# Kernel tuning notes

Hardware: AMD Instinct MI355X
Metric: run time of the kernel (lower is better)

Reference implementation:

```python
import jax, jax.numpy as jnp
import numpy as np

B, N, M, D, H, K, V = 2, 2048, 2048, 1024, 16, 64, 64
MAX_WAVELENGTH = 10000
SCALE_FACTOR = 1.0


def rope(x, positions, max_wavelength, scale_factor):
    # x: [b, s, h, k]; positions: [b, s] int
    head_dim = x.shape[-1]
    fraction = 2.0 * jnp.arange(head_dim // 2, dtype=x.dtype) / head_dim
    timescale = jnp.asarray(max_wavelength, x.dtype) ** fraction            # [k/2]
    # scaled positions -> phase per (b, s, 1 head bcast, k/2)
    phase = (positions.astype(x.dtype) / scale_factor)[:, :, None, None] / timescale  # [b,s,1,k/2]
    sin, cos = jnp.sin(phase), jnp.cos(phase)
    x1, x2 = jnp.split(x, 2, axis=-1)
    return jnp.concatenate([x1 * cos - x2 * sin, x2 * cos + x1 * sin], axis=-1)


def setup_inputs() -> dict:
    key = jax.random.key(0)
    ks = jax.random.split(key, 8)
    scale = 1.0 / np.sqrt(D)  # keep logits numerically sane with random params
    inp = {
        "query": jax.random.normal(ks[0], (B, N, D), jnp.float32),
        "q_positions": jnp.broadcast_to(jnp.arange(N, dtype=jnp.int32), (B, N)),
        "key": jax.random.normal(ks[1], (B, M, D), jnp.float32),
        "k_positions": jnp.broadcast_to(jnp.arange(M, dtype=jnp.int32), (B, M)),
        "value": jax.random.normal(ks[2], (B, M, D), jnp.float32),
        "mask": jnp.ones((1, 1, N, M), dtype=bool),
        "P_q": jax.random.normal(ks[3], (H, D, K), jnp.float32) * scale,
        "P_k": jax.random.normal(ks[4], (H, D, K), jnp.float32) * scale,
        "P_v": jax.random.normal(ks[5], (H, D, V), jnp.float32) * scale,
        "P_o": jax.random.normal(ks[6], (H, D, V), jnp.float32) * scale,
    }
    return inp


def reference(query, q_positions, key, k_positions, value, mask, P_q, P_k, P_v, P_o):
    q = jnp.einsum('bnd,hdk->bnhk', query, P_q)
    k = jnp.einsum('bmd,hdk->bmhk', key, P_k)
    v = jnp.einsum('bmd,hdv->bmhv', value, P_v)
    q = rope(q, q_positions, MAX_WAVELENGTH, SCALE_FACTOR)
    k = rope(k, k_positions, MAX_WAVELENGTH, SCALE_FACTOR)
    logits = jnp.einsum('bnhk,bmhk->bhnm', q, k)
    if mask is not None:
        logits = jnp.where(mask, logits, -jnp.inf)
    weights = jax.nn.softmax(logits, axis=-1)
    o = jnp.einsum('bhnm,bmhv->bnhv', weights, v)
    return jnp.einsum('bnhv,hdv->bnd', o, P_o)
```

## Files before the change

kernel.cpp:

```cpp
#include <hip/hip_runtime.h>
#include <hip/hip_bf16.h>
#include <math.h>

#define B_ 2
#define N_ 2048
#define M_ 2048
#define D_ 1024
#define H_ 16


typedef _Float16 f16;
typedef f16  f16x4 __attribute__((ext_vector_type(4)));
typedef f16  f16x8 __attribute__((ext_vector_type(8)));
typedef float f32x4  __attribute__((ext_vector_type(4)));
typedef float f32x16 __attribute__((ext_vector_type(16)));

#define MFMA16(a, b, c) __builtin_amdgcn_mfma_f32_16x16x32_f16((a), (b), (c), 0, 0, 0)
#define MFMA32(a, b, c) __builtin_amdgcn_mfma_f32_32x32x16_f16((a), (b), (c), 0, 0, 0)
#define LDST 72

__global__ __launch_bounds__(256) void prep_all(
    const float* __restrict__ Pq, const float* __restrict__ Pk,
    const float* __restrict__ Pv, const float* __restrict__ Po,
    const int* __restrict__ qpos, const int* __restrict__ kpos,
    f16* __restrict__ Ptq, f16* __restrict__ Ptk, f16* __restrict__ Ptv,
    f16* __restrict__ Wo, float2* __restrict__ tabq, float2* __restrict__ tabk)
{
  __shared__ float Ts[64][65];
  const int z = blockIdx.y, x = blockIdx.x, tid = threadIdx.x;
  if (z < 3) {
    if (x >= 256) return;
    const float* P = (z == 0) ? Pq : (z == 1) ? Pk : Pv;
    f16* Pt = (z == 0) ? Ptq : (z == 1) ? Ptk : Ptv;
    const int d0 = (x & 15) * 64, h = x >> 4;
    #pragma unroll
    for (int it = 0; it < 4; ++it) {
      int fi = tid + 256 * it;
      int dr = fi >> 4, c4 = (fi & 15) << 2;
      float4 v = *(const float4*)(P + ((size_t)h * D_ + d0 + dr) * 64 + c4);
      Ts[dr][c4+0] = v.x; Ts[dr][c4+1] = v.y; Ts[dr][c4+2] = v.z; Ts[dr][c4+3] = v.w;
    }
    __syncthreads();
    const int c = tid >> 2, dp = (tid & 3) * 16;
    f16x8 w0, w1;
    #pragma unroll
    for (int i = 0; i < 8; ++i) { w0[i] = (f16)Ts[dp + i][c]; w1[i] = (f16)Ts[dp + 8 + i][c]; }
    f16* dst = Pt + ((size_t)h * 64 + c) * D_ + d0 + dp;
    *(f16x8*)dst = w0;
    *(f16x8*)(dst + 8) = w1;
  } else if (z == 3) {
    int e = (x * 256 + tid) * 4;
    if (e >= H_ * D_ * 64) return;
    int h = e >> 16, d = (e >> 6) & 1023, v = e & 63;
    float4 xx = *(const float4*)(Po + e);
    f16x4 w = {(f16)xx.x, (f16)xx.y, (f16)xx.z, (f16)xx.w};
    *(f16x4*)&Wo[(size_t)d * 1024 + h * 64 + v] = w;
  } else {
    if (x >= 512) return;
    int idx = x * 256 + tid;
    int r = idx >> 5, c = idx & 31;
    const int* pos = (z == 4) ? qpos : kpos;
    float2* tab = (z == 4) ? tabq : tabk;
    float fpos = (float)pos[r];
    float inv_ts = exp2f(-(float)c * 0.4152410118609203f);
    float ph = fpos * inv_ts, sn, cs;
    sincosf(ph, &sn, &cs);
    tab[idx] = make_float2(cs, sn);
  }
}

__global__ __launch_bounds__(256) void gemm_fused(
    const float* __restrict__ Aq, const float* __restrict__ Ak,
    const float* __restrict__ Av,
    const f16* __restrict__ Bq, const f16* __restrict__ Bk,
    const f16* __restrict__ Bv,
    const float2* __restrict__ tabq, const float2* __restrict__ tabk,
    f16* __restrict__ dq, f16* __restrict__ dk, f16* __restrict__ dv)
{
  __shared__ f16 As[128 * LDST];
  __shared__ f16 Bs[128 * LDST];
  const int tid = threadIdx.x, lane = tid & 63, wave = tid >> 6;
  const int quad = lane >> 4, l16 = lane & 15;
  const int col0 = blockIdx.x * 128, row0 = blockIdx.y * 128;
  const int op = blockIdx.z;
  const int wr = (wave >> 1) * 64, wc = (wave & 1) * 64;

  const float* A  = (op == 0) ? Aq : (op == 1) ? Ak : Av;
  const f16*  Bt  = (op == 0) ? Bq : (op == 1) ? Bk : Bv;

  f32x4 acc[4][4] = {};
  float4 apre[8];
  f16x8  bpre[4];

  #pragma unroll
  for (int it = 0; it < 8; ++it) {
    int fi = tid + 256 * it;
    int row = fi >> 4, c4 = (fi & 15) << 2;
    apre[it] = *(const float4*)(A + (size_t)(row0 + row) * 1024 + c4);
  }
  #pragma unroll
  for (int it = 0; it < 4; ++it) {
    int fi = tid + 256 * it;
    int row = fi >> 3, c8 = (fi & 7) * 8;
    bpre[it] = *(const f16x8*)(Bt + (size_t)(col0 + row) * 1024 + c8);
  }

  for (int k0 = 0; k0 < 1024; k0 += 64) {
    __syncthreads();
    #pragma unroll
    for (int it = 0; it < 8; ++it) {
      int fi = tid + 256 * it;
      int row = fi >> 4, c4 = (fi & 15) << 2;
      f16x4 hv = {(f16)apre[it].x, (f16)apre[it].y, (f16)apre[it].z, (f16)apre[it].w};
      *(f16x4*)&As[row * LDST + c4] = hv;
    }
    #pragma unroll
    for (int it = 0; it < 4; ++it) {
      int fi = tid + 256 * it;
      int row = fi >> 3, c8 = (fi & 7) * 8;
      *(f16x8*)&Bs[row * LDST + c8] = bpre[it];
    }
    __syncthreads();
    if (k0 + 64 < 1024) {
      #pragma unroll
      for (int it = 0; it < 8; ++it) {
        int fi = tid + 256 * it;
        int row = fi >> 4, c4 = (fi & 15) << 2;
        apre[it] = *(const float4*)(A + (size_t)(row0 + row) * 1024 + k0 + 64 + c4);
      }
      #pragma unroll
      for (int it = 0; it < 4; ++it) {
        int fi = tid + 256 * it;
        int row = fi >> 3, c8 = (fi & 7) * 8;
        bpre[it] = *(const f16x8*)(Bt + (size_t)(col0 + row) * 1024 + k0 + 64 + c8);
      }
    }
    #pragma unroll
    for (int ks = 0; ks < 2; ++ks) {
      f16x8 af[4], bf[4];
      #pragma unroll
      for (int i = 0; i < 4; ++i)
        af[i] = *(const f16x8*)&As[(wr + i * 16 + l16) * LDST + ks * 32 + quad * 8];
      #pragma unroll
      for (int j = 0; j < 4; ++j)
        bf[j] = *(const f16x8*)&Bs[(wc + j * 16 + l16) * LDST + ks * 32 + quad * 8];
      #pragma unroll
      for (int i = 0; i < 4; ++i)
        #pragma unroll
        for (int j = 0; j < 4; ++j)
          acc[i][j] = MFMA16(af[i], bf[j], acc[i][j]);
    }
  }

  if (op == 2) {
    #pragma unroll
    for (int i = 0; i < 4; ++i) {
      int r = row0 + wr + i * 16 + quad * 4;
      int b = r >> 11, s = r & 2047;
      #pragma unroll
      for (int j = 0; j < 4; ++j) {
        int col = col0 + wc + j * 16 + l16;
        int h = col >> 6, v = col & 63;
        f16x4 w = {(f16)acc[i][j][0], (f16)acc[i][j][1],
                   (f16)acc[i][j][2], (f16)acc[i][j][3]};
        *(f16x4*)&dv[((size_t)(b * H_ + h) * 64 + v) * 2048 + s] = w;
      }
    }
  } else {
    const float2* tab = (op == 0) ? tabq : tabk;
    f16* oq = (op == 0) ? dq : dk;
    #pragma unroll
    for (int i = 0; i < 4; ++i) {
      #pragma unroll
      for (int reg = 0; reg < 4; ++reg) {
        int r = row0 + wr + i * 16 + quad * 4 + reg;
        int b = r >> 11, s = r & 2047;
        #pragma unroll
        for (int j = 0; j < 2; ++j) {
          int col = col0 + wc + j * 16 + l16;
          int h = col >> 6, c = col & 63;
          float2 cs = tab[r * 32 + c];
          float x1 = acc[i][j][reg], x2 = acc[i][j + 2][reg];
          size_t base = ((size_t)(b * H_ + h) * 2048 + s) * 64;
          oq[base + c]      = (f16)(x1 * cs.x - x2 * cs.y);
          oq[base + c + 32] = (f16)(x2 * cs.x + x1 * cs.y);
        }
      }
    }
  }
}

__global__ __launch_bounds__(256) void flash5(
    const f16* __restrict__ q, const f16* __restrict__ k,
    const f16* __restrict__ vt, f16* __restrict__ o)
{
  __shared__ f16 Ks[64 * LDST];
  __shared__ f16 Vts[64 * LDST];
  __shared__ f16 Ps[4][32 * LDST];

  const int tid = threadIdx.x, lane = tid & 63, wave = tid >> 6;
  const int L = lane >> 5, nl = lane & 31;
  const int n0 = blockIdx.x * 128;
  const int h = blockIdx.y, b = blockIdx.z;

  const f16* qb = q  + (size_t)(b * H_ + h) * N_ * 64;
  const f16* kb = k  + (size_t)(b * H_ + h) * M_ * 64;
  const f16* vb = vt + (size_t)(b * H_ + h) * 64 * M_;

  f16x8 qf[4];
  #pragma unroll
  for (int g = 0; g < 4; ++g)
    qf[g] = *(const f16x8*)(qb + (size_t)(n0 + wave * 32 + nl) * 64 + g * 16 + L * 8);

  f32x16 acc[2] = {};
  float mst = -INFINITY;
  float lst = 0.f;
  const float L2E = 1.4426950408889634f;

  const int srow = tid >> 2, soff = (tid & 3) * 16;
  f16* psw = Ps[wave];

  f16x8 kp0 = *(const f16x8*)(kb + (size_t)srow * 64 + soff);
  f16x8 kp1 = *(const f16x8*)(kb + (size_t)srow * 64 + soff + 8);
  f16x8 vp0 = *(const f16x8*)(vb + (size_t)srow * M_ + soff);
  f16x8 vp1 = *(const f16x8*)(vb + (size_t)srow * M_ + soff + 8);

  for (int m0 = 0; m0 < M_; m0 += 64) {
    __syncthreads();
    *(f16x8*)&Ks[srow * LDST + soff]      = kp0;
    *(f16x8*)&Ks[srow * LDST + soff + 8]  = kp1;
    *(f16x8*)&Vts[srow * LDST + soff]     = vp0;
    *(f16x8*)&Vts[srow * LDST + soff + 8] = vp1;
    __syncthreads();
    if (m0 + 64 < M_) {
      kp0 = *(const f16x8*)(kb + (size_t)(m0 + 64 + srow) * 64 + soff);
      kp1 = *(const f16x8*)(kb + (size_t)(m0 + 64 + srow) * 64 + soff + 8);
      vp0 = *(const f16x8*)(vb + (size_t)srow * M_ + m0 + 64 + soff);
      vp1 = *(const f16x8*)(vb + (size_t)srow * M_ + m0 + 64 + soff + 8);
    }

    f32x16 s[2] = {};
    #pragma unroll
    for (int u = 0; u < 2; ++u)
      #pragma unroll
      for (int g = 0; g < 4; ++g) {
        f16x8 af = *(const f16x8*)&Ks[(u * 32 + nl) * LDST + g * 16 + L * 8];
        s[u] = MFMA32(af, qf[g], s[u]);
      }

    float mx = s[0][0];
    #pragma unroll
    for (int u = 0; u < 2; ++u)
      #pragma unroll
      for (int r = 0; r < 16; ++r) mx = fmaxf(mx, s[u][r]);
    mx = fmaxf(mx, __shfl_xor(mx, 32));
    float m_new = fmaxf(mst, mx * L2E);
    bool chg = (m_new > mst);
    if (__ballot(chg)) {
      float alpha = exp2f(mst - m_new);
      #pragma unroll
      for (int u = 0; u < 2; ++u)
        #pragma unroll
        for (int r = 0; r < 16; ++r) acc[u][r] *= alpha;
      lst *= alpha;
    }
    mst = m_new;

    float sum = 0.f;
    float p[2][16];
    #pragma unroll
    for (int u = 0; u < 2; ++u)
      #pragma unroll
      for (int r = 0; r < 16; ++r) {
        float pv = exp2f(s[u][r] * L2E - m_new);
        p[u][r] = pv;
        sum += pv;
      }
    sum += __shfl_xor(sum, 32);
    lst += sum;

    #pragma unroll
    for (int u = 0; u < 2; ++u)
      #pragma unroll
      for (int rq = 0; rq < 4; ++rq) {
        f16x4 w = {(f16)p[u][rq * 4 + 0], (f16)p[u][rq * 4 + 1],
                   (f16)p[u][rq * 4 + 2], (f16)p[u][rq * 4 + 3]};
        *(f16x4*)&psw[nl * LDST + u * 32 + 8 * rq + 4 * L] = w;
      }
    f16x8 pb[4];
    #pragma unroll
    for (int g = 0; g < 4; ++g)
      pb[g] = *(const f16x8*)&psw[nl * LDST + g * 16 + L * 8];

    #pragma unroll
    for (int u = 0; u < 2; ++u)
      #pragma unroll
      for (int g = 0; g < 4; ++g) {
        f16x8 vf = *(const f16x8*)&Vts[(u * 32 + nl) * LDST + g * 16 + L * 8];
        acc[u] = MFMA32(vf, pb[g], acc[u]);
      }
  }

  float invl = 1.0f / lst;
  f16* ob = o + ((size_t)(b * N_ + n0 + wave * 32 + nl) * 1024) + h * 64;
  #pragma unroll
  for (int u = 0; u < 2; ++u)
    #pragma unroll
    for (int rq = 0; rq < 4; ++rq) {
      f16x4 w = {(f16)(acc[u][rq * 4 + 0] * invl), (f16)(acc[u][rq * 4 + 1] * invl),
                 (f16)(acc[u][rq * 4 + 2] * invl), (f16)(acc[u][rq * 4 + 3] * invl)};
      *(f16x4*)&ob[u * 32 + 8 * rq + 4 * L] = w;
    }
}

__global__ __launch_bounds__(256) void gemm_out(
    const f16* __restrict__ A, const f16* __restrict__ Bt,
    float* __restrict__ out)
{
  __shared__ f16 As[128 * LDST];
  __shared__ f16 Bs[64 * LDST];
  const int tid = threadIdx.x, lane = tid & 63, wave = tid >> 6;
  const int quad = lane >> 4, l16 = lane & 15;
  const int col0 = blockIdx.x * 64, row0 = blockIdx.y * 128;
  const int wr = (wave >> 1) * 64, wc = (wave & 1) * 32;

  f32x4 acc[4][2] = {};
  f16x8 apre[4], bpre[2];

  #pragma unroll
  for (int it = 0; it < 4; ++it) {
    int fi = tid + 256 * it;
    int row = fi >> 3, c8 = (fi & 7) * 8;
    apre[it] = *(const f16x8*)(A + (size_t)(row0 + row) * 1024 + c8);
  }
  #pragma unroll
  for (int it = 0; it < 2; ++it) {
    int fi = tid + 256 * it;
    int row = fi >> 3, c8 = (fi & 7) * 8;
    bpre[it] = *(const f16x8*)(Bt + (size_t)(col0 + row) * 1024 + c8);
  }

  for (int k0 = 0; k0 < 1024; k0 += 64) {
    __syncthreads();
    #pragma unroll
    for (int it = 0; it < 4; ++it) {
      int fi = tid + 256 * it;
      int row = fi >> 3, c8 = (fi & 7) * 8;
      *(f16x8*)&As[row * LDST + c8] = apre[it];
    }
    #pragma unroll
    for (int it = 0; it < 2; ++it) {
      int fi = tid + 256 * it;
      int row = fi >> 3, c8 = (fi & 7) * 8;
      *(f16x8*)&Bs[row * LDST + c8] = bpre[it];
    }
    __syncthreads();
    if (k0 + 64 < 1024) {
      #pragma unroll
      for (int it = 0; it < 4; ++it) {
        int fi = tid + 256 * it;
        int row = fi >> 3, c8 = (fi & 7) * 8;
        apre[it] = *(const f16x8*)(A + (size_t)(row0 + row) * 1024 + k0 + 64 + c8);
      }
      #pragma unroll
      for (int it = 0; it < 2; ++it) {
        int fi = tid + 256 * it;
        int row = fi >> 3, c8 = (fi & 7) * 8;
        bpre[it] = *(const f16x8*)(Bt + (size_t)(col0 + row) * 1024 + k0 + 64 + c8);
      }
    }
    #pragma unroll
    for (int ks = 0; ks < 2; ++ks) {
      f16x8 af[4], bf[2];
      #pragma unroll
      for (int i = 0; i < 4; ++i)
        af[i] = *(const f16x8*)&As[(wr + i * 16 + l16) * LDST + ks * 32 + quad * 8];
      #pragma unroll
      for (int j = 0; j < 2; ++j)
        bf[j] = *(const f16x8*)&Bs[(wc + j * 16 + l16) * LDST + ks * 32 + quad * 8];
      #pragma unroll
      for (int i = 0; i < 4; ++i)
        #pragma unroll
        for (int j = 0; j < 2; ++j)
          acc[i][j] = MFMA16(af[i], bf[j], acc[i][j]);
    }
  }

  #pragma unroll
  for (int i = 0; i < 4; ++i)
    #pragma unroll
    for (int j = 0; j < 2; ++j)
      #pragma unroll
      for (int reg = 0; reg < 4; ++reg)
        out[(size_t)(row0 + wr + i * 16 + quad * 4 + reg) * 1024 +
            col0 + wc + j * 16 + l16] = acc[i][j][reg];
}

extern "C" void kernel_launch(void* const* d_in, const int* in_sizes, int n_in,
                              void* d_out, int out_size, void* d_ws, size_t ws_size,
                              hipStream_t stream) {
  (void)in_sizes; (void)n_in; (void)out_size; (void)ws_size;
  const float* query = (const float*)d_in[0];
  const int*   qpos  = (const int*)d_in[1];
  const float* key   = (const float*)d_in[2];
  const int*   kpos  = (const int*)d_in[3];
  const float* value = (const float*)d_in[4];
  const float* Pq = (const float*)d_in[6];
  const float* Pk = (const float*)d_in[7];
  const float* Pv = (const float*)d_in[8];
  const float* Po = (const float*)d_in[9];
  float* out = (float*)d_out;

  const size_t pm = (size_t)1024 * 1024;
  const size_t em = (size_t)B_ * H_ * 2048 * 64;
  f16* Ptq = (f16*)d_ws;
  f16* Ptk = Ptq + pm;
  f16* Ptv = Ptk + pm;
  f16* Wo  = Ptv + pm;
  f16* q_ws  = Wo + pm;
  f16* k_ws  = q_ws + em;
  f16* vt_ws = k_ws + em;
  f16* o_ws  = vt_ws + em;
  float2* tabq = (float2*)(o_ws + em);
  float2* tabk = tabq + (size_t)4096 * 32;

  dim3 blk(256);
  prep_all<<<dim3(1024, 6), blk, 0, stream>>>(
      Pq, Pk, Pv, Po, qpos, kpos, Ptq, Ptk, Ptv, Wo, tabq, tabk);

  gemm_fused<<<dim3(8, 32, 3), blk, 0, stream>>>(
      query, key, value, Ptq, Ptk, Ptv, tabq, tabk, q_ws, k_ws, vt_ws);

  flash5<<<dim3(N_ / 128, H_, B_), blk, 0, stream>>>(q_ws, k_ws, vt_ws, o_ws);

  gemm_out<<<dim3(16, 32), blk, 0, stream>>>(o_ws, Wo, out);
}
```

Measured before the change: 270.7 us.

## Keep softmax probabilities in registers via permlane swap, add lazy rescale

The flash attention kernel no longer round-trips the P tile through per-wave LDS. It packs probabilities to f16 pairs with cvt_pkrtz and rearranges them across lane halves with v_permlane32_swap into the MFMA B-operand layout. It also adds a lazy max rescale that only updates the running max when it grows by more than 8 in log2 units, tree-reduces max and sum, wraps the MFMA sections in s_setprio, and sets launch bounds for two blocks per CU. Removing the LDS traffic and the conditional rescales should shorten the inner loop. The cost is reliance on the exact lane layout and some extra headroom risk in the fp16 probabilities.

```diff
diff --git a/kernel.cpp b/kernel.cpp
--- a/kernel.cpp
+++ b/kernel.cpp
@@ -18,6 +18,11 @@
 #define MFMA16(a, b, c) __builtin_amdgcn_mfma_f32_16x16x32_f16((a), (b), (c), 0, 0, 0)
 #define MFMA32(a, b, c) __builtin_amdgcn_mfma_f32_32x32x16_f16((a), (b), (c), 0, 0, 0)
 #define LDST 72
+
+static __device__ __forceinline__ unsigned int pk2(float a, float b) {
+  auto h = __builtin_amdgcn_cvt_pkrtz(a, b);
+  return __builtin_bit_cast(unsigned int, h);
+}
 
 __global__ __launch_bounds__(256) void prep_all(
     const float* __restrict__ Pq, const float* __restrict__ Pk,
@@ -190,13 +195,12 @@
   }
 }
 
-__global__ __launch_bounds__(256) void flash5(
+__global__ __launch_bounds__(256, 2) void flash6(
     const f16* __restrict__ q, const f16* __restrict__ k,
     const f16* __restrict__ vt, f16* __restrict__ o)
 {
   __shared__ f16 Ks[64 * LDST];
   __shared__ f16 Vts[64 * LDST];
-  __shared__ f16 Ps[4][32 * LDST];
 
   const int tid = threadIdx.x, lane = tid & 63, wave = tid >> 6;
   const int L = lane >> 5, nl = lane & 31;
@@ -218,7 +222,6 @@
   const float L2E = 1.4426950408889634f;
 
   const int srow = tid >> 2, soff = (tid & 3) * 16;
-  f16* psw = Ps[wave];
 
   f16x8 kp0 = *(const f16x8*)(kb + (size_t)srow * 64 + soff);
   f16x8 kp1 = *(const f16x8*)(kb + (size_t)srow * 64 + soff + 8);
@@ -240,6 +243,7 @@
     }
 
     f32x16 s[2] = {};
+    __builtin_amdgcn_s_setprio(1);
     #pragma unroll
     for (int u = 0; u < 2; ++u)
       #pragma unroll
@@ -247,58 +251,77 @@
         f16x8 af = *(const f16x8*)&Ks[(u * 32 + nl) * LDST + g * 16 + L * 8];
         s[u] = MFMA32(af, qf[g], s[u]);
       }
-
-    float mx = s[0][0];
-    #pragma unroll
-    for (int u = 0; u < 2; ++u)
-      #pragma unroll
-      for (int r = 0; r < 16; ++r) mx = fmaxf(mx, s[u][r]);
-    mx = fmaxf(mx, __shfl_xor(mx, 32));
-    float m_new = fmaxf(mst, mx * L2E);
-    bool chg = (m_new > mst);
-    if (__ballot(chg)) {
+    __builtin_amdgcn_s_setprio(0);
+
+    float tm[16];
+    #pragma unroll
+    for (int r = 0; r < 16; ++r) tm[r] = fmaxf(s[0][r], s[1][r]);
+    #pragma unroll
+    for (int st = 8; st >= 1; st >>= 1)
+      #pragma unroll
+      for (int r = 0; r < st; ++r) tm[r] = fmaxf(tm[r], tm[r + st]);
+    float mx = fmaxf(tm[0], __shfl_xor(tm[0], 32));
+    float mx2 = mx * L2E;
+    float m_new = fmaxf(mst, mx2);
+
+    if (!__all(mx2 - mst <= 8.0f)) {
       float alpha = exp2f(mst - m_new);
       #pragma unroll
       for (int u = 0; u < 2; ++u)
         #pragma unroll
         for (int r = 0; r < 16; ++r) acc[u][r] *= alpha;
       lst *= alpha;
-    }
-    mst = m_new;
-
-    float sum = 0.f;
+      mst = m_new;
+    }
+
     float p[2][16];
     #pragma unroll
     for (int u = 0; u < 2; ++u)
       #pragma unroll
-      for (int r = 0; r < 16; ++r) {
-        float pv = exp2f(s[u][r] * L2E - m_new);
-        p[u][r] = pv;
-        sum += pv;
-      }
+      for (int r = 0; r < 16; ++r)
+        p[u][r] = exp2f(s[u][r] * L2E - mst);
+
+    float ts[16];
+    #pragma unroll
+    for (int r = 0; r < 16; ++r) ts[r] = p[0][r] + p[1][r];
+    #pragma unroll
+    for (int st = 8; st >= 1; st >>= 1)
+      #pragma unroll
+      for (int r = 0; r < st; ++r) ts[r] += ts[r + st];
+    float sum = ts[0];
     sum += __shfl_xor(sum, 32);
     lst += sum;
 
+    unsigned int qw[2][4][2];
     #pragma unroll
     for (int u = 0; u < 2; ++u)
       #pragma unroll
       for (int rq = 0; rq < 4; ++rq) {
-        f16x4 w = {(f16)p[u][rq * 4 + 0], (f16)p[u][rq * 4 + 1],
-                   (f16)p[u][rq * 4 + 2], (f16)p[u][rq * 4 + 3]};
-        *(f16x4*)&psw[nl * LDST + u * 32 + 8 * rq + 4 * L] = w;
-      }
-    f16x8 pb[4];
-    #pragma unroll
-    for (int g = 0; g < 4; ++g)
-      pb[g] = *(const f16x8*)&psw[nl * LDST + g * 16 + L * 8];
-
+        qw[u][rq][0] = pk2(p[u][rq * 4 + 0], p[u][rq * 4 + 1]);
+        qw[u][rq][1] = pk2(p[u][rq * 4 + 2], p[u][rq * 4 + 3]);
+      }
+    union PBu { unsigned int w[4]; f16x8 v; } pb[4];
+    #pragma unroll
+    for (int u = 0; u < 2; ++u)
+      #pragma unroll
+      for (int gg = 0; gg < 2; ++gg)
+        #pragma unroll
+        for (int w = 0; w < 2; ++w) {
+          unsigned int a = qw[u][2 * gg][w], bb = qw[u][2 * gg + 1][w];
+          asm volatile("v_permlane32_swap_b32 %0, %1" : "+v"(a), "+v"(bb));
+          pb[2 * u + gg].w[w]     = a;
+          pb[2 * u + gg].w[2 + w] = bb;
+        }
+
+    __builtin_amdgcn_s_setprio(1);
     #pragma unroll
     for (int u = 0; u < 2; ++u)
       #pragma unroll
       for (int g = 0; g < 4; ++g) {
         f16x8 vf = *(const f16x8*)&Vts[(u * 32 + nl) * LDST + g * 16 + L * 8];
-        acc[u] = MFMA32(vf, pb[g], acc[u]);
-      }
+        acc[u] = MFMA32(vf, pb[g].v, acc[u]);
+      }
+    __builtin_amdgcn_s_setprio(0);
   }
 
   float invl = 1.0f / lst;
@@ -431,7 +454,7 @@
   gemm_fused<<<dim3(8, 32, 3), blk, 0, stream>>>(
       query, key, value, Ptq, Ptk, Ptv, tabq, tabk, q_ws, k_ws, vt_ws);
 
-  flash5<<<dim3(N_ / 128, H_, B_), blk, 0, stream>>>(q_ws, k_ws, vt_ws, o_ws);
+  flash6<<<dim3(N_ / 128, H_, B_), blk, 0, stream>>>(q_ws, k_ws, vt_ws, o_ws);
 
   gemm_out<<<dim3(16, 32), blk, 0, stream>>>(o_ws, Wo, out);
 }
```

New measurement: 265.7 us. About the same (-1.9%).
